# Kernel optimization log

Hardware: AMD Instinct MI355X
Metric: run time of the kernel (lower is better)

The kernel has to match this reference:

```python
import jax, jax.numpy as jnp
import numpy as np

MAX_DEPTH = 6
NUM_TREES = 64
LEAF_DIMS = 128
D_IN = 512
BATCH = 4096
N_INTERNAL = 2 ** MAX_DEPTH - 1  # 63
N_LEAVES = 2 ** MAX_DEPTH        # 64


def setup_inputs() -> dict:
    key = jax.random.key(0)
    ks = jax.random.split(key, 4)
    x = jax.random.normal(ks[0], (BATCH, D_IN), dtype=jnp.float32)
    # Stacked internal-node dense layers, node i at index i (level order, node_index ordering)
    W = jax.random.normal(ks[1], (N_INTERNAL, D_IN, NUM_TREES), dtype=jnp.float32) / np.sqrt(D_IN)
    b = jnp.zeros((N_INTERNAL, NUM_TREES), dtype=jnp.float32)
    leaf_weight = jax.random.normal(ks[2], (N_LEAVES, LEAF_DIMS, NUM_TREES), dtype=jnp.float32)
    gates = jax.random.normal(ks[3], (N_LEAVES, LEAF_DIMS, NUM_TREES), dtype=jnp.float32)
    return {"x": x, "W": W, "b": b, "leaf_weight": leaf_weight, "gates": gates}


def reference(x, W, b, leaf_weight, gates):
    # All internal-node gating probabilities in one batched matmul:
    # g[b, n, t] = sigmoid(x[b] @ W[n] + b[n])  for every internal node n, tree t
    g = jax.nn.sigmoid(jnp.einsum('bd,ndt->bnt', x, W) + b[None, :, :])  # [B, 63, T]

    B = x.shape[0]
    T = W.shape[-1]
    # Path probability to each leaf, built level by level.
    # Level l has 2^l nodes at internal indices [2^l - 1, 2^(l+1) - 2];
    # interleaving (left=p*g, right=p*(1-g)) matches node_index child ordering.
    p = jnp.ones((B, 1, T), dtype=x.dtype)
    for level in range(MAX_DEPTH):
        start = 2 ** level - 1
        n_lvl = 2 ** level
        gl = g[:, start:start + n_lvl, :]                  # [B, n_lvl, T]
        children = jnp.stack([p * gl, p * (1.0 - gl)], axis=2)  # [B, n_lvl, 2, T]
        p = children.reshape(B, 2 * n_lvl, T)
    # p: [B, n_leaves, T] leaf path probabilities

    # Softmax mixture-of-experts gate over trees, then weighted leaf mixture:
    # out[b, d] = sum_{l, t} p[b, l, t] * leaf_weight[l, d, t] * softmax(gates, -1)[l, d, t]
    w = leaf_weight * jax.nn.softmax(gates, axis=-1)  # [L, D, T]
    out = jnp.einsum('blt,ldt->bd', p, w)
    return out
```

## Files before the change

kernel.cpp:

```cpp
#include <hip/hip_runtime.h>
#include <stdint.h>

#define BATCH 4096
#define DIN   512
#define NT    64
#define NL    64
#define LD    128

typedef __attribute__((ext_vector_type(8))) short bf16x8;
typedef __attribute__((ext_vector_type(8))) _Float16 f16x8;
typedef __attribute__((ext_vector_type(4))) float f32x4;

typedef const __attribute__((address_space(1))) unsigned char* gcp_t;
typedef __attribute__((address_space(3))) unsigned char* lp_t;

__device__ __forceinline__ void gl_lds16(const void* g, void* l) {
  __builtin_amdgcn_global_load_lds((gcp_t)g, (lp_t)l, 16, 0, 0);
}

__device__ __forceinline__ unsigned pk_bf16(float a, float b) {
  union { float f; unsigned u; } ua, ub;
  ua.f = a; ub.f = b;
  return __builtin_amdgcn_perm(ub.u + 0x8000u, ua.u + 0x8000u, 0x07060302u);
}

__global__ __launch_bounds__(256) void prep_all_k(
    const float* __restrict__ x, const float* __restrict__ W,
    const float* __restrict__ gates, const float* __restrict__ lw,
    unsigned short* __restrict__ xb, unsigned short* __restrict__ Wt,
    unsigned short* __restrict__ Wv2, float* __restrict__ out) {
  __shared__ float smem[12288];
  const int bx = blockIdx.x;
  const int tid = threadIdx.x;

  if (bx < 2048) {
    int i = bx * 256 + tid;
    float4 v = ((const float4*)x)[i];
    uint2 o;
    o.x = pk_bf16(v.x, v.y);
    o.y = pk_bf16(v.z, v.w);
    ((uint2*)xb)[i] = o;
  } else if (bx < 2304) {
    int bb = bx - 2048;
    int n = bb >> 2, d0 = (bb & 3) * 128;
    float* buf = smem;
    if (n < 63) {
      for (int it = 0; it < 32; ++it) {
        int idx = it * 256 + tid;
        buf[idx] = W[n * 32768 + (d0 + (idx >> 6)) * 64 + (idx & 63)];
      }
    }
    __syncthreads();
    int t = tid >> 2, q = tid & 3;
    unsigned vals[16];
    #pragma unroll
    for (int j = 0; j < 16; ++j) {
      float va = (n < 63) ? buf[(q * 32 + 2 * j) * 64 + t] : 0.0f;
      float vb = (n < 63) ? buf[(q * 32 + 2 * j + 1) * 64 + t] : 0.0f;
      vals[j] = (n < 63) ? pk_bf16(va, vb) : 0u;
    }
    uint4* dst = (uint4*)(Wt + t * 32768 + n * 512 + d0 + q * 32);
    const uint4* src = (const uint4*)vals;
    dst[0] = src[0]; dst[1] = src[1]; dst[2] = src[2]; dst[3] = src[3];
  } else if (bx < 2432) {
    int d = bx - 2304;
    float* gb = smem;
    float* lb = smem + 4096;
    float* wv = smem + 8192;
    for (int it = 0; it < 16; ++it) {
      int idx = it * 256 + tid;
      int l = idx >> 6;
      int ga = l * 8192 + d * 64 + (idx & 63);
      gb[idx] = gates[ga];
      lb[idx] = lw[ga];
    }
    __syncthreads();
    int wave = tid >> 6, lane = tid & 63;
    for (int l = wave; l < 64; l += 4) {
      float v = gb[l * 64 + lane];
      float mx = v;
      for (int m = 32; m >= 1; m >>= 1) mx = fmaxf(mx, __shfl_xor(mx, m));
      float e = __expf(v - mx);
      float s = e;
      for (int m = 32; m >= 1; m >>= 1) s += __shfl_xor(s, m);
      wv[l * 64 + lane] = lb[l * 64 + lane] * e / s;
    }
    __syncthreads();
    #pragma unroll
    for (int c = 0; c < 2; ++c) {
      int k0 = tid * 16 + c * 8;
      unsigned o[4];
      #pragma unroll
      for (int j = 0; j < 4; ++j) {
        int ka = k0 + 2 * j, kb = k0 + 2 * j + 1;
        o[j] = pk_bf16(wv[(ka & 63) * 64 + (ka >> 6)], wv[(kb & 63) * 64 + (kb >> 6)]);
      }
      *(uint4*)(Wv2 + (long)d * 4096 + k0) = *(const uint4*)o;
    }
  } else {
    float4 z = {0.f, 0.f, 0.f, 0.f};
    int base = (bx - 2432) * 256 + tid;
    float4* o4 = (float4*)out;
    #pragma unroll
    for (int k = 0; k < 16; ++k)
      o4[k * 8192 + base] = z;
  }
}

__global__ __launch_bounds__(512, 4) void gemm1_tree_k(
    const unsigned short* __restrict__ xb,
    const unsigned short* __restrict__ Wt,
    const float* __restrict__ bias,
    unsigned short* __restrict__ P)
{
  __shared__ __align__(16) char smem[73728];
  unsigned short* AsB = (unsigned short*)smem;
  unsigned short* BsB = (unsigned short*)(smem + 49152);
  _Float16* gbuf = (_Float16*)smem;

  const int tid = threadIdx.x;
  const int wave = tid >> 6, lane = tid & 63;

  const int lin = blockIdx.x;
  const int rr = lin & 7, kq = lin >> 3;
  const int b0 = ((kq & 3) | ((rr & 3) << 2)) * 256;
  const int t0 = ((kq >> 2) | ((rr >> 2) << 4)) * 2;

  const int wm = (wave >> 1) * 64, wn = (wave & 1) * 64;
  const int mrow = lane & 15, kg = lane >> 4;
  const int slot = (kg ^ ((mrow >> 1) & 3)) * 8;

  float bv[4];
  #pragma unroll
  for (int j = 0; j < 4; ++j) {
    int n = j * 16 + mrow;
    bv[j] = (n < 63) ? bias[n * 64 + t0 + (wave & 1)] : 0.0f;
  }

  const f32x4 zero = {0.f, 0.f, 0.f, 0.f};
  f32x4 acc[4][4];
  #pragma unroll
  for (int i = 0; i < 4; ++i)
    #pragma unroll
    for (int j = 0; j < 4; ++j) acc[i][j] = zero;

  const int g0 = tid;
  const int g1 = tid + 512;
  const int c0 = ((g0 & 3) ^ ((g0 >> 3) & 3)) * 8;
  const int c1 = ((g1 & 3) ^ ((g1 >> 3) & 3)) * 8;
  const unsigned short* Ag0 = xb + (long)(b0 + (g0 >> 2)) * 512 + c0;
  const unsigned short* Ag1 = xb + (long)(b0 + (g1 >> 2)) * 512 + c1;
  const unsigned short* Bg0 = Wt + (long)(t0 * 64 + (g0 >> 2)) * 512 + c0;
  const int lofsA0 = wave * 512;
  const int lofsA1 = wave * 512 + 4096;
  const int lofsB  = wave * 512;

  gl_lds16(Ag0, AsB + lofsA0);
  gl_lds16(Ag1, AsB + lofsA1);
  gl_lds16(Bg0, BsB + lofsB);
  gl_lds16(Ag0 + 32, AsB + 8192 + lofsA0);
  gl_lds16(Ag1 + 32, AsB + 8192 + lofsA1);
  gl_lds16(Bg0 + 32, BsB + 4096 + lofsB);

  for (int it = 0; it < 16; ++it) {
    const int bufA = (it % 3) * 8192;
    const int bufB = (it % 3) * 4096;
    if (it < 15) {
      asm volatile("s_waitcnt vmcnt(3) lgkmcnt(0)" ::: "memory");
    } else {
      asm volatile("s_waitcnt vmcnt(0) lgkmcnt(0)" ::: "memory");
    }
    asm volatile("s_barrier" ::: "memory");

    if (it < 14) {
      const int kk = (it + 2) * 32;
      const int nA = ((it + 2) % 3) * 8192;
      const int nB = ((it + 2) % 3) * 4096;
      gl_lds16(Ag0 + kk, AsB + nA + lofsA0);
      gl_lds16(Ag1 + kk, AsB + nA + lofsA1);
      gl_lds16(Bg0 + kk, BsB + nB + lofsB);
    }

    bf16x8 fa[4], fb[4];
    #pragma unroll
    for (int i = 0; i < 4; ++i)
      fa[i] = *(const bf16x8*)(AsB + bufA + (wm + i * 16 + mrow) * 32 + slot);
    #pragma unroll
    for (int j = 0; j < 4; ++j)
      fb[j] = *(const bf16x8*)(BsB + bufB + (wn + j * 16 + mrow) * 32 + slot);
    #pragma unroll
    for (int i = 0; i < 4; ++i)
      #pragma unroll
      for (int j = 0; j < 4; ++j)
        acc[i][j] = __builtin_amdgcn_mfma_f32_16x16x32_bf16(fa[i], fb[j], acc[i][j], 0, 0, 0);
  }

  __syncthreads();

  #pragma unroll
  for (int i = 0; i < 4; ++i)
    #pragma unroll
    for (int j = 0; j < 4; ++j) {
      int col = wn + j * 16 + mrow;
      int oct = col >> 3, sub = col & 7;
      #pragma unroll
      for (int r = 0; r < 4; ++r) {
        int row = wm + i * 16 + kg * 4 + r;
        float z = acc[i][j][r] + bv[j];
        gbuf[row * 128 + ((oct ^ (row & 15)) << 3) + sub] =
            (_Float16)__builtin_amdgcn_rcpf(1.0f + __expf(-z));
      }
    }
  __syncthreads();

  {
    const int row = tid >> 1, tr = tid & 1;
    const _Float16* grow = gbuf + row * 128;
    const int rx = row & 15;
    float g[63];
    #pragma unroll
    for (int c = 0; c < 8; ++c) {
      f16x8 gv = *(const f16x8*)(grow + (((tr * 8 + c) ^ rx) << 3));
      #pragma unroll
      for (int j = 0; j < 8; ++j) {
        int n = c * 8 + j;
        if (n < 63) g[n] = (float)gv[j];
      }
    }
    float P3[8];
    {
      float a0 = g[0],            a1 = 1.0f - g[0];
      float c0_ = a0 * g[1],      c1_ = a0 * (1.0f - g[1]);
      float c2_ = a1 * g[2],      c3_ = a1 * (1.0f - g[2]);
      P3[0] = c0_ * g[3];  P3[1] = c0_ * (1.0f - g[3]);
      P3[2] = c1_ * g[4];  P3[3] = c1_ * (1.0f - g[4]);
      P3[4] = c2_ * g[5];  P3[5] = c2_ * (1.0f - g[5]);
      P3[6] = c3_ * g[6];  P3[7] = c3_ * (1.0f - g[6]);
    }
    unsigned short* prow = P + (long)(b0 + row) * 4096 + (t0 + tr) * 64;
    #pragma unroll
    for (int o = 0; o < 8; ++o) {
      float g3 = g[7 + o];
      float q0 = P3[o] * g3, q1 = P3[o] * (1.0f - g3);
      float g4a = g[15 + 2 * o], g4b = g[16 + 2 * o];
      float r0 = q0 * g4a, r1 = q0 * (1.0f - g4a);
      float r2 = q1 * g4b, r3 = q1 * (1.0f - g4b);
      unsigned ou[4];
      #pragma unroll
      for (int h = 0; h < 4; ++h) {
        float g5 = g[31 + 4 * o + h];
        float rr2 = (h == 0) ? r0 : (h == 1) ? r1 : (h == 2) ? r2 : r3;
        ou[h] = pk_bf16(rr2 * g5, rr2 * (1.0f - g5));
      }
      *(uint4*)(prow + o * 8) = *(const uint4*)ou;
    }
  }
}

__global__ __launch_bounds__(256, 4) void gemm2_k(
    const unsigned short* __restrict__ P,
    const unsigned short* __restrict__ Wv2,
    float* __restrict__ out)
{
  __shared__ unsigned short AsB[3][64 * 32];
  __shared__ unsigned short BsB[3][64 * 32];
  const int tid = threadIdx.x;
  const int wave = tid >> 6, lane = tid & 63;
  const int b0 = blockIdx.x * 64;
  const int k0 = blockIdx.y * 1024;
  const int n0 = blockIdx.z * 64;

  const f32x4 zero = {0.f, 0.f, 0.f, 0.f};
  f32x4 acc[2][2];
  #pragma unroll
  for (int i = 0; i < 2; ++i)
    #pragma unroll
    for (int j = 0; j < 2; ++j) acc[i][j] = zero;

  const int c0 = ((tid & 3) ^ ((tid >> 3) & 3)) * 8;
  const unsigned short* Ag0 = P   + (long)(b0 + (tid >> 2)) * 4096 + k0 + c0;
  const unsigned short* Bg0 = Wv2 + (long)(n0 + (tid >> 2)) * 4096 + k0 + c0;
  const int lofs = wave * 512;

  const int wm = (wave >> 1) * 32, wn = (wave & 1) * 32;
  const int mrow = lane & 15, kg = lane >> 4;
  const int slot = (kg ^ ((mrow >> 1) & 3)) * 8;

  gl_lds16(Ag0,      AsB[0] + lofs);
  gl_lds16(Bg0,      BsB[0] + lofs);
  gl_lds16(Ag0 + 32, AsB[1] + lofs);
  gl_lds16(Bg0 + 32, BsB[1] + lofs);

  for (int it = 0; it < 32; ++it) {
    const int buf = it % 3;
    if (it < 31) {
      asm volatile("s_waitcnt vmcnt(2) lgkmcnt(0)" ::: "memory");
    } else {
      asm volatile("s_waitcnt vmcnt(0) lgkmcnt(0)" ::: "memory");
    }
    asm volatile("s_barrier" ::: "memory");

    if (it < 30) {
      const int kk = (it + 2) * 32;
      const int nb = (it + 2) % 3;
      gl_lds16(Ag0 + kk, AsB[nb] + lofs);
      gl_lds16(Bg0 + kk, BsB[nb] + lofs);
    }

    bf16x8 fa[2], fb[2];
    #pragma unroll
    for (int i = 0; i < 2; ++i)
      fa[i] = *(const bf16x8*)(AsB[buf] + (wm + i * 16 + mrow) * 32 + slot);
    #pragma unroll
    for (int j = 0; j < 2; ++j)
      fb[j] = *(const bf16x8*)(BsB[buf] + (wn + j * 16 + mrow) * 32 + slot);
    #pragma unroll
    for (int i = 0; i < 2; ++i)
      #pragma unroll
      for (int j = 0; j < 2; ++j)
        acc[i][j] = __builtin_amdgcn_mfma_f32_16x16x32_bf16(fa[i], fb[j], acc[i][j], 0, 0, 0);
  }

  #pragma unroll
  for (int i = 0; i < 2; ++i)
    #pragma unroll
    for (int j = 0; j < 2; ++j) {
      int col = n0 + wn + j * 16 + mrow;
      #pragma unroll
      for (int r = 0; r < 4; ++r) {
        int row = wm + i * 16 + kg * 4 + r;
        atomicAdd(&out[(long)(b0 + row) * 128 + col], acc[i][j][r]);
      }
    }
}

extern "C" void kernel_launch(void* const* d_in, const int* in_sizes, int n_in,
                              void* d_out, int out_size, void* d_ws, size_t ws_size,
                              hipStream_t stream) {
  const float* x     = (const float*)d_in[0];
  const float* W     = (const float*)d_in[1];
  const float* b     = (const float*)d_in[2];
  const float* lw    = (const float*)d_in[3];
  const float* gates = (const float*)d_in[4];
  float* out = (float*)d_out;

  char* ws = (char*)d_ws;
  unsigned short* xb  = (unsigned short*)(ws);
  unsigned short* Wt  = (unsigned short*)(ws + (4l  << 20));
  unsigned short* Wv2 = (unsigned short*)(ws + (8l  << 20));
  unsigned short* P   = (unsigned short*)(ws + (16l << 20));

  hipLaunchKernelGGL(prep_all_k,   dim3(2464), dim3(256), 0, stream,
                     x, W, gates, lw, xb, Wt, Wv2, out);
  hipLaunchKernelGGL(gemm1_tree_k, dim3(512),  dim3(512), 0, stream, xb, Wt, b, P);
  hipLaunchKernelGGL(gemm2_k,      dim3(64, 4, 2), dim3(256), 0, stream, P, Wv2, out);
}
```

Before: 130.2 us.

## Fuse leaf-probability GEMM into gating GEMM kernel, dropping P round trip

Merges the second GEMM into the gating/tree kernel. Each block now covers 128 batch rows by 4 trees, stores its bf16 leaf probabilities in LDS, and multiplies them directly with Wv2 loaded from global memory, then atomically adds into the output. This removes the 32MB P intermediate write and read plus one kernel launch. In exchange there are more atomics per output element (16 tree groups instead of 4 K-splits), and the Wv2 fragments are read from global without prefetching.

Result: no change. 131.6 us (+1.1%).

```diff
diff --git a/kernel.cpp b/kernel.cpp
--- a/kernel.cpp
+++ b/kernel.cpp
@@ -107,34 +107,39 @@
   }
 }
 
-__global__ __launch_bounds__(512, 4) void gemm1_tree_k(
+__global__ __launch_bounds__(512, 4) void gemm1_fused_k(
     const unsigned short* __restrict__ xb,
     const unsigned short* __restrict__ Wt,
     const float* __restrict__ bias,
-    unsigned short* __restrict__ P)
+    const unsigned short* __restrict__ Wv2,
+    float* __restrict__ out)
 {
   __shared__ __align__(16) char smem[73728];
   unsigned short* AsB = (unsigned short*)smem;
-  unsigned short* BsB = (unsigned short*)(smem + 49152);
+  unsigned short* BsB = (unsigned short*)(smem + 24576);
   _Float16* gbuf = (_Float16*)smem;
+  unsigned short* plds = (unsigned short*)smem;
 
   const int tid = threadIdx.x;
   const int wave = tid >> 6, lane = tid & 63;
 
   const int lin = blockIdx.x;
-  const int rr = lin & 7, kq = lin >> 3;
-  const int b0 = ((kq & 3) | ((rr & 3) << 2)) * 256;
-  const int t0 = ((kq >> 2) | ((rr >> 2) << 4)) * 2;
-
-  const int wm = (wave >> 1) * 64, wn = (wave & 1) * 64;
+  const int xcd = lin & 7, idx = lin >> 3;
+  const int bt = (xcd >> 1) * 8 + (idx >> 3);
+  const int tq = (xcd & 1) * 8 + (idx & 7);
+  const int b0 = bt << 7;
+  const int n0 = tq << 8;
+
+  const int wm = (wave >> 2) << 6;
+  const int wn = (wave & 3) << 6;
   const int mrow = lane & 15, kg = lane >> 4;
   const int slot = (kg ^ ((mrow >> 1) & 3)) * 8;
 
   float bv[4];
   #pragma unroll
   for (int j = 0; j < 4; ++j) {
-    int n = j * 16 + mrow;
-    bv[j] = (n < 63) ? bias[n * 64 + t0 + (wave & 1)] : 0.0f;
+    int node = j * 16 + mrow;
+    bv[j] = (node < 63) ? bias[node * 64 + tq * 4 + (wave & 3)] : 0.0f;
   }
 
   const f32x4 zero = {0.f, 0.f, 0.f, 0.f};
@@ -144,27 +149,22 @@
     #pragma unroll
     for (int j = 0; j < 4; ++j) acc[i][j] = zero;
 
-  const int g0 = tid;
-  const int g1 = tid + 512;
-  const int c0 = ((g0 & 3) ^ ((g0 >> 3) & 3)) * 8;
-  const int c1 = ((g1 & 3) ^ ((g1 >> 3) & 3)) * 8;
-  const unsigned short* Ag0 = xb + (long)(b0 + (g0 >> 2)) * 512 + c0;
-  const unsigned short* Ag1 = xb + (long)(b0 + (g1 >> 2)) * 512 + c1;
-  const unsigned short* Bg0 = Wt + (long)(t0 * 64 + (g0 >> 2)) * 512 + c0;
-  const int lofsA0 = wave * 512;
-  const int lofsA1 = wave * 512 + 4096;
-  const int lofsB  = wave * 512;
-
-  gl_lds16(Ag0, AsB + lofsA0);
-  gl_lds16(Ag1, AsB + lofsA1);
-  gl_lds16(Bg0, BsB + lofsB);
-  gl_lds16(Ag0 + 32, AsB + 8192 + lofsA0);
-  gl_lds16(Ag1 + 32, AsB + 8192 + lofsA1);
-  gl_lds16(Bg0 + 32, BsB + 4096 + lofsB);
+  const int cA = ((tid & 3) ^ ((tid >> 3) & 3)) * 8;
+  const unsigned short* Ag0 = xb + (long)(b0 + (tid >> 2)) * 512 + cA;
+  const unsigned short* Bg0 = Wt + (long)(n0 + (tid >> 2)) * 512 + cA;
+  const unsigned short* Bg1 = Wt + (long)(n0 + 128 + (tid >> 2)) * 512 + cA;
+  const int ldst = tid * 8;
+
+  gl_lds16(Ag0, AsB + ldst);
+  gl_lds16(Bg0, BsB + ldst);
+  gl_lds16(Bg1, BsB + ldst + 4096);
+  gl_lds16(Ag0 + 32, AsB + 4096 + ldst);
+  gl_lds16(Bg0 + 32, BsB + 8192 + ldst);
+  gl_lds16(Bg1 + 32, BsB + 8192 + ldst + 4096);
 
   for (int it = 0; it < 16; ++it) {
-    const int bufA = (it % 3) * 8192;
-    const int bufB = (it % 3) * 4096;
+    const int bufA = (it % 3) * 4096;
+    const int bufB = (it % 3) * 8192;
     if (it < 15) {
       asm volatile("s_waitcnt vmcnt(3) lgkmcnt(0)" ::: "memory");
     } else {
@@ -174,11 +174,11 @@
 
     if (it < 14) {
       const int kk = (it + 2) * 32;
-      const int nA = ((it + 2) % 3) * 8192;
-      const int nB = ((it + 2) % 3) * 4096;
-      gl_lds16(Ag0 + kk, AsB + nA + lofsA0);
-      gl_lds16(Ag1 + kk, AsB + nA + lofsA1);
-      gl_lds16(Bg0 + kk, BsB + nB + lofsB);
+      const int nA = ((it + 2) % 3) * 4096;
+      const int nB = ((it + 2) % 3) * 8192;
+      gl_lds16(Ag0 + kk, AsB + nA + ldst);
+      gl_lds16(Bg0 + kk, BsB + nB + ldst);
+      gl_lds16(Bg1 + kk, BsB + nB + ldst + 4096);
     }
 
     bf16x8 fa[4], fb[4];
@@ -202,25 +202,24 @@
     #pragma unroll
     for (int j = 0; j < 4; ++j) {
       int col = wn + j * 16 + mrow;
-      int oct = col >> 3, sub = col & 7;
+      int ch = col >> 3, sub = col & 7;
       #pragma unroll
       for (int r = 0; r < 4; ++r) {
         int row = wm + i * 16 + kg * 4 + r;
         float z = acc[i][j][r] + bv[j];
-        gbuf[row * 128 + ((oct ^ (row & 15)) << 3) + sub] =
+        gbuf[row * 256 + (((ch ^ (row & 31)) << 3) | sub)] =
             (_Float16)__builtin_amdgcn_rcpf(1.0f + __expf(-z));
       }
     }
   __syncthreads();
 
   {
-    const int row = tid >> 1, tr = tid & 1;
-    const _Float16* grow = gbuf + row * 128;
-    const int rx = row & 15;
+    const int row = tid >> 2, tree = tid & 3;
+    const int rx = row & 31;
     float g[63];
     #pragma unroll
     for (int c = 0; c < 8; ++c) {
-      f16x8 gv = *(const f16x8*)(grow + (((tr * 8 + c) ^ rx) << 3));
+      f16x8 gv = *(const f16x8*)(gbuf + row * 256 + (((tree * 8 + c) ^ rx) << 3));
       #pragma unroll
       for (int j = 0; j < 8; ++j) {
         int n = c * 8 + j;
@@ -237,7 +236,7 @@
       P3[4] = c2_ * g[5];  P3[5] = c2_ * (1.0f - g[5]);
       P3[6] = c3_ * g[6];  P3[7] = c3_ * (1.0f - g[6]);
     }
-    unsigned short* prow = P + (long)(b0 + row) * 4096 + (t0 + tr) * 64;
+    unsigned pk32[32];
     #pragma unroll
     for (int o = 0; o < 8; ++o) {
       float g3 = g[7 + o];
@@ -245,93 +244,63 @@
       float g4a = g[15 + 2 * o], g4b = g[16 + 2 * o];
       float r0 = q0 * g4a, r1 = q0 * (1.0f - g4a);
       float r2 = q1 * g4b, r3 = q1 * (1.0f - g4b);
-      unsigned ou[4];
       #pragma unroll
       for (int h = 0; h < 4; ++h) {
         float g5 = g[31 + 4 * o + h];
         float rr2 = (h == 0) ? r0 : (h == 1) ? r1 : (h == 2) ? r2 : r3;
-        ou[h] = pk_bf16(rr2 * g5, rr2 * (1.0f - g5));
-      }
-      *(uint4*)(prow + o * 8) = *(const uint4*)ou;
-    }
-  }
-}
-
-__global__ __launch_bounds__(256, 4) void gemm2_k(
-    const unsigned short* __restrict__ P,
-    const unsigned short* __restrict__ Wv2,
-    float* __restrict__ out)
-{
-  __shared__ unsigned short AsB[3][64 * 32];
-  __shared__ unsigned short BsB[3][64 * 32];
-  const int tid = threadIdx.x;
-  const int wave = tid >> 6, lane = tid & 63;
-  const int b0 = blockIdx.x * 64;
-  const int k0 = blockIdx.y * 1024;
-  const int n0 = blockIdx.z * 64;
-
-  const f32x4 zero = {0.f, 0.f, 0.f, 0.f};
-  f32x4 acc[2][2];
-  #pragma unroll
-  for (int i = 0; i < 2; ++i)
-    #pragma unroll
-    for (int j = 0; j < 2; ++j) acc[i][j] = zero;
-
-  const int c0 = ((tid & 3) ^ ((tid >> 3) & 3)) * 8;
-  const unsigned short* Ag0 = P   + (long)(b0 + (tid >> 2)) * 4096 + k0 + c0;
-  const unsigned short* Bg0 = Wv2 + (long)(n0 + (tid >> 2)) * 4096 + k0 + c0;
-  const int lofs = wave * 512;
-
-  const int wm = (wave >> 1) * 32, wn = (wave & 1) * 32;
-  const int mrow = lane & 15, kg = lane >> 4;
-  const int slot = (kg ^ ((mrow >> 1) & 3)) * 8;
-
-  gl_lds16(Ag0,      AsB[0] + lofs);
-  gl_lds16(Bg0,      BsB[0] + lofs);
-  gl_lds16(Ag0 + 32, AsB[1] + lofs);
-  gl_lds16(Bg0 + 32, BsB[1] + lofs);
-
-  for (int it = 0; it < 32; ++it) {
-    const int buf = it % 3;
-    if (it < 31) {
-      asm volatile("s_waitcnt vmcnt(2) lgkmcnt(0)" ::: "memory");
-    } else {
-      asm volatile("s_waitcnt vmcnt(0) lgkmcnt(0)" ::: "memory");
-    }
-    asm volatile("s_barrier" ::: "memory");
-
-    if (it < 30) {
-      const int kk = (it + 2) * 32;
-      const int nb = (it + 2) % 3;
-      gl_lds16(Ag0 + kk, AsB[nb] + lofs);
-      gl_lds16(Bg0 + kk, BsB[nb] + lofs);
-    }
-
-    bf16x8 fa[2], fb[2];
-    #pragma unroll
-    for (int i = 0; i < 2; ++i)
-      fa[i] = *(const bf16x8*)(AsB[buf] + (wm + i * 16 + mrow) * 32 + slot);
-    #pragma unroll
-    for (int j = 0; j < 2; ++j)
-      fb[j] = *(const bf16x8*)(BsB[buf] + (wn + j * 16 + mrow) * 32 + slot);
-    #pragma unroll
-    for (int i = 0; i < 2; ++i)
+        pk32[o * 4 + h] = pk_bf16(rr2 * g5, rr2 * (1.0f - g5));
+      }
+    }
+    __syncthreads();
+
+    #pragma unroll
+    for (int g2 = 0; g2 < 8; ++g2) {
+      int ksub = tree * 2 + (g2 >> 2);
+      int c = g2 & 3;
+      uint4 v = {pk32[g2 * 4], pk32[g2 * 4 + 1], pk32[g2 * 4 + 2], pk32[g2 * 4 + 3]};
+      *(uint4*)(plds + ksub * 4096 + row * 32 + ((c ^ ((row >> 1) & 3)) << 3)) = v;
+    }
+  }
+  __syncthreads();
+
+  {
+    const int wm2 = (wave >> 2) << 6;
+    const int wn2 = (wave & 3) << 5;
+    f32x4 acc2[4][2];
+    #pragma unroll
+    for (int i = 0; i < 4; ++i)
+      #pragma unroll
+      for (int j = 0; j < 2; ++j) acc2[i][j] = zero;
+
+    #pragma unroll
+    for (int kq = 0; kq < 8; ++kq) {
+      bf16x8 fa2[4], fbg[2];
       #pragma unroll
       for (int j = 0; j < 2; ++j)
-        acc[i][j] = __builtin_amdgcn_mfma_f32_16x16x32_bf16(fa[i], fb[j], acc[i][j], 0, 0, 0);
-  }
-
-  #pragma unroll
-  for (int i = 0; i < 2; ++i)
-    #pragma unroll
-    for (int j = 0; j < 2; ++j) {
-      int col = n0 + wn + j * 16 + mrow;
-      #pragma unroll
-      for (int r = 0; r < 4; ++r) {
-        int row = wm + i * 16 + kg * 4 + r;
-        atomicAdd(&out[(long)(b0 + row) * 128 + col], acc[i][j][r]);
-      }
-    }
+        fbg[j] = *(const bf16x8*)(Wv2 + (long)(wn2 + j * 16 + mrow) * 4096 +
+                                  tq * 256 + kq * 32 + kg * 8);
+      #pragma unroll
+      for (int i = 0; i < 4; ++i)
+        fa2[i] = *(const bf16x8*)(plds + kq * 4096 + (wm2 + i * 16 + mrow) * 32 + slot);
+      #pragma unroll
+      for (int i = 0; i < 4; ++i)
+        #pragma unroll
+        for (int j = 0; j < 2; ++j)
+          acc2[i][j] = __builtin_amdgcn_mfma_f32_16x16x32_bf16(fa2[i], fbg[j], acc2[i][j], 0, 0, 0);
+    }
+
+    #pragma unroll
+    for (int i = 0; i < 4; ++i)
+      #pragma unroll
+      for (int j = 0; j < 2; ++j) {
+        int col = wn2 + j * 16 + mrow;
+        #pragma unroll
+        for (int r = 0; r < 4; ++r) {
+          int row = wm2 + i * 16 + kg * 4 + r;
+          atomicAdd(&out[(long)(b0 + row) * 128 + col], acc2[i][j][r]);
+        }
+      }
+  }
 }
 
 extern "C" void kernel_launch(void* const* d_in, const int* in_sizes, int n_in,
@@ -348,10 +317,9 @@
   unsigned short* xb  = (unsigned short*)(ws);
   unsigned short* Wt  = (unsigned short*)(ws + (4l  << 20));
   unsigned short* Wv2 = (unsigned short*)(ws + (8l  << 20));
-  unsigned short* P   = (unsigned short*)(ws + (16l << 20));
-
-  hipLaunchKernelGGL(prep_all_k,   dim3(2464), dim3(256), 0, stream,
+
+  hipLaunchKernelGGL(prep_all_k,    dim3(2464), dim3(256), 0, stream,
                      x, W, gates, lw, xb, Wt, Wv2, out);
-  hipLaunchKernelGGL(gemm1_tree_k, dim3(512),  dim3(512), 0, stream, xb, Wt, b, P);
-  hipLaunchKernelGGL(gemm2_k,      dim3(64, 4, 2), dim3(256), 0, stream, P, Wv2, out);
-}
+  hipLaunchKernelGGL(gemm1_fused_k, dim3(512),  dim3(512), 0, stream,
+                     xb, Wt, b, Wv2, out);
+}
```
